# Performance work log

Hardware: AMD Instinct MI355X
Metric: run time of the kernel (lower is better)

## Reference

```python
import jax, jax.numpy as jnp
import numpy as np

N = 100000   # nodes
E = 3200000  # directed edges
F_IN = 128   # data.num_node_features
H = 16       # hidden
C = 2        # output classes (hard-coded in module)


def _glorot(key, fan_in, fan_out):
    s = jnp.sqrt(6.0 / (fan_in + fan_out)).astype(jnp.float32)
    return jax.random.uniform(key, (fan_in, fan_out), jnp.float32, -s, s)


def setup_inputs() -> dict:
    key = jax.random.key(0)
    ks = jax.random.split(key, 5)
    x = jax.random.normal(ks[0], (N, F_IN), jnp.float32)
    edge_index = jax.random.randint(ks[1], (2, E), 0, N, dtype=jnp.int64)
    return {
        "x": x,
        "edge_index": edge_index,
        "W1": _glorot(ks[2], F_IN, H), "b1": jnp.zeros((H,), jnp.float32),
        "W2": _glorot(ks[3], H, H),    "b2": jnp.zeros((H,), jnp.float32),
        "W3": _glorot(ks[4], H, C),    "b3": jnp.zeros((C,), jnp.float32),
    }


def _gcn_conv(x, W, b, src, dst, norm, n):
    # PyG GCNConv: linear transform, then normalized gather -> scatter-add, + bias
    h = x @ W                                   # [N, out]
    msg = h[src] * norm[:, None]                # [E+N, out] gather over source nodes
    out = jax.ops.segment_sum(msg, dst, num_segments=n)  # scatter-add at targets
    return out + b


def reference(x, edge_index, W1, b1, W2, b2, W3, b3):
    n = x.shape[0]
    loop = jnp.arange(n, dtype=edge_index.dtype)
    src = jnp.concatenate([edge_index[0], loop])  # add self-loops (PyG default)
    dst = jnp.concatenate([edge_index[1], loop])
    # symmetric normalization: deg^{-1/2}[src] * deg^{-1/2}[dst], deg = in-degree w/ self-loops
    deg = jax.ops.segment_sum(jnp.ones(src.shape, jnp.float32), dst, num_segments=n)
    dis = jnp.where(deg > 0, jax.lax.rsqrt(jnp.maximum(deg, 1.0)), 0.0)
    norm = dis[src] * dis[dst]
    # dropout is identity in eval mode
    h = jax.nn.relu(_gcn_conv(x, W1, b1, src, dst, norm, n))
    h = jax.nn.relu(_gcn_conv(h, W2, b2, src, dst, norm, n))
    h = _gcn_conv(h, W3, b3, src, dst, norm, n)
    return jax.nn.log_softmax(h, axis=1)
```

## Files before the change

kernel.cpp:

```cpp
#include <hip/hip_runtime.h>
#include <math.h>

#define NSB   512
#define BSH   8
#define BKN   256
#define ESMAX 6272
#define NBSMX 128

typedef _Float16 h8  __attribute__((ext_vector_type(8)));
typedef _Float16 h4  __attribute__((ext_vector_type(4)));
typedef _Float16 h2v __attribute__((ext_vector_type(2)));

__device__ inline int wave_scan_incl(int v) {
    int lane = threadIdx.x & 63;
#pragma unroll
    for (int d = 1; d < 64; d <<= 1) {
        int t = __shfl_up(v, d, 64);
        if (lane >= d) v += t;
    }
    return v;
}


__global__ void k_scan1(const int* __restrict__ in, int* __restrict__ out,
                        int* __restrict__ bsum, int n) {
    __shared__ int wsum[4];
    int base = blockIdx.x * 2048 + threadIdx.x * 8;
    int v[8];
    int ts = 0;
#pragma unroll
    for (int j = 0; j < 8; j++) {
        int idx = base + j;
        v[j] = ts;
        ts += (idx < n) ? in[idx] : 0;
    }
    int inc = wave_scan_incl(ts);
    int wid = threadIdx.x >> 6;
    if ((threadIdx.x & 63) == 63) wsum[wid] = inc;
    __syncthreads();
    int wofs = 0;
#pragma unroll
    for (int w = 0; w < 4; w++) wofs += (w < wid) ? wsum[w] : 0;
    int excl = inc - ts + wofs;
#pragma unroll
    for (int j = 0; j < 8; j++) {
        int idx = base + j;
        if (idx < n) out[idx] = excl + v[j];
    }
    if (threadIdx.x == 255) bsum[blockIdx.x] = excl + ts;
}

__device__ inline void scan_bsum(const int* __restrict__ bsum, int nbs,
                                 int* sb, int* wsumB) {
    int tid = threadIdx.x;
    int v = (tid < nbs) ? bsum[tid] : 0;
    int inc = wave_scan_incl(v);
    int wid = tid >> 6;
    if (tid < NBSMX && (tid & 63) == 63) wsumB[wid] = inc;
    __syncthreads();
    if (tid < nbs) {
        int wofs = 0;
#pragma unroll
        for (int w = 0; w < 2; w++) wofs += (w < wid) ? wsumB[w] : 0;
        sb[tid] = inc - v + wofs;
    }
    __syncthreads();
}


__global__ void k_hist(const int* __restrict__ dst, int* __restrict__ hist,
                       int e, int nbuck, int es) {
    __shared__ int h[512];
    for (int i = threadIdx.x; i < 512; i += blockDim.x) h[i] = 0;
    __syncthreads();
    int lo = blockIdx.x * es;
    int hi = min(lo + es, e);
    for (int i = lo + threadIdx.x; i < hi; i += blockDim.x)
        atomicAdd(&h[dst[i] >> BSH], 1);
    __syncthreads();
    for (int i = threadIdx.x; i < nbuck; i += blockDim.x)
        hist[(size_t)i * gridDim.x + blockIdx.x] = h[i];
}

__global__ void k_bucket(const int* __restrict__ src, const int* __restrict__ dst,
                         const int* __restrict__ hist, const int* __restrict__ offs,
                         const int* __restrict__ bsum, unsigned* __restrict__ col,
                         int e, int nbuck, int es, int nbs) {
    __shared__ unsigned sorted[ESMAX];
    __shared__ unsigned char sbuck[ESMAX];
    __shared__ int lofE[512], lcur[512], soff[512];
    __shared__ int sb[NBSMX];
    __shared__ int wsum[8];
    int tid = threadIdx.x;
    scan_bsum(bsum, nbs, sb, wsum);
    int lc = 0;
    if (tid < nbuck) {
        size_t idx = (size_t)tid * gridDim.x + blockIdx.x;
        lc = hist[idx];
        soff[tid] = offs[idx] + sb[idx >> 11];
    }
    int inc = wave_scan_incl(lc);
    int wid = tid >> 6;
    if ((tid & 63) == 63) wsum[wid] = inc;
    __syncthreads();
    int wofs = 0;
#pragma unroll
    for (int w = 0; w < 8; w++) wofs += (w < wid) ? wsum[w] : 0;
    int excl = inc - lc + wofs;
    lofE[tid] = excl;
    lcur[tid] = excl;
    __syncthreads();
    int lo = blockIdx.x * es;
    int hi = min(lo + es, e);
    for (int i = lo + tid; i < hi; i += 512) {
        int d = dst[i];
        int b = d >> BSH;
        int p = atomicAdd(&lcur[b], 1);
        sorted[p] = ((unsigned)src[i] << BSH) | (unsigned)(d & (BKN - 1));
        sbuck[p] = (unsigned char)(b & 255);
    }
    __syncthreads();
    int cnt_ = hi - lo;
    int split = (nbuck > 256) ? lofE[256] : 0x7fffffff;
    for (int i = tid; i < cnt_; i += 512) {
        int b = sbuck[i] | ((i >= split) ? 256 : 0);
        col[soff[b] + (i - lofE[b])] = sorted[i];
    }
}

__global__ void k_sort(const unsigned* __restrict__ col, const int* __restrict__ offs,
                       const int* __restrict__ bsum, int* __restrict__ col2,
                       int* __restrict__ rs, float* __restrict__ dis,
                       int n, int e, int nbuck, int nbs) {
    __shared__ int cnt[BKN];
    __shared__ int cur[BKN];
    __shared__ int sb[NBSMX];
    __shared__ int wsum[4];
    int tid = threadIdx.x;
    int b = blockIdx.x;
    scan_bsum(bsum, nbs, sb, wsum);
    size_t i0 = (size_t)b * NSB;
    int lo = offs[i0] + sb[i0 >> 11];
    int hi = e;
    if (b + 1 < nbuck) {
        size_t i1 = (size_t)(b + 1) * NSB;
        hi = offs[i1] + sb[i1 >> 11];
    }
    if (tid < BKN) cnt[tid] = 0;
    __syncthreads();
    for (int i = lo + tid; i < hi; i += 512)
        atomicAdd(&cnt[col[i] & (BKN - 1u)], 1);
    __syncthreads();
    int c = (tid < BKN) ? cnt[tid] : 0;
    int inc = wave_scan_incl(c);
    int wid = tid >> 6;
    if (tid < BKN && (tid & 63) == 63) wsum[wid] = inc;
    __syncthreads();
    if (tid < BKN) {
        int wofs = 0;
#pragma unroll
        for (int w = 0; w < 4; w++) wofs += (w < wid) ? wsum[w] : 0;
        int excl = inc - c + wofs;
        cur[tid] = lo + excl;
        int node = (b << BSH) + tid;
        if (node < n) {
            rs[node] = lo + excl;
            dis[node] = rsqrtf((float)(c + 1));
        }
    }
    if (b == 0 && tid == 0) rs[n] = e;
    __syncthreads();
    for (int i = lo + tid; i < hi; i += 512) {
        unsigned v = col[i];
        int pos = atomicAdd(&cur[v & (BKN - 1u)], 1);
        col2[pos] = (int)(v >> BSH);
    }
}


__global__ __launch_bounds__(512) void k_linear1s(
        const float* __restrict__ x, const float* __restrict__ W,
        const float* __restrict__ dis, _Float16* __restrict__ hs, int n) {
    __shared__ float sW[2048];
    int tid = threadIdx.x;
    for (int i = tid; i < 2048; i += 512) sW[i] = W[i];
    __syncthreads();
    int cg = tid & 3;
    int kg = (tid >> 2) & 7;
    int nl = tid >> 5;
    float wr[16][4];
#pragma unroll
    for (int j = 0; j < 16; j++)
#pragma unroll
        for (int cc = 0; cc < 4; cc++)
            wr[j][cc] = sW[(kg * 16 + j) * 16 + cg * 4 + cc];
    int nodeBase = blockIdx.x * 128 + nl;
    for (int it = 0; it < 8; it++) {
        int node = nodeBase + it * 16;
        float a0 = 0.f, a1 = 0.f, a2 = 0.f, a3 = 0.f;
        if (node < n) {
            const float4* xr = (const float4*)(x + (size_t)node * 128 + kg * 16);
#pragma unroll
            for (int j4 = 0; j4 < 4; j4++) {
                float4 xv = xr[j4];
                float xs0 = xv.x, xs1 = xv.y, xs2 = xv.z, xs3 = xv.w;
                int j = j4 * 4;
                a0 += xs0 * wr[j][0] + xs1 * wr[j+1][0] + xs2 * wr[j+2][0] + xs3 * wr[j+3][0];
                a1 += xs0 * wr[j][1] + xs1 * wr[j+1][1] + xs2 * wr[j+2][1] + xs3 * wr[j+3][1];
                a2 += xs0 * wr[j][2] + xs1 * wr[j+1][2] + xs2 * wr[j+2][2] + xs3 * wr[j+3][2];
                a3 += xs0 * wr[j][3] + xs1 * wr[j+1][3] + xs2 * wr[j+2][3] + xs3 * wr[j+3][3];
            }
        }
#pragma unroll
        for (int m = 4; m <= 16; m <<= 1) {
            a0 += __shfl_xor(a0, m);
            a1 += __shfl_xor(a1, m);
            a2 += __shfl_xor(a2, m);
            a3 += __shfl_xor(a3, m);
        }
        if (kg == 0 && node < n) {
            float d = dis[node];
            h4 o;
            o[0] = (_Float16)(a0 * d);
            o[1] = (_Float16)(a1 * d);
            o[2] = (_Float16)(a2 * d);
            o[3] = (_Float16)(a3 * d);
            *((h4*)(hs + (size_t)node * 16 + cg * 4)) = o;
        }
    }
}


__global__ void k_pullA(const _Float16* __restrict__ hs, const int* __restrict__ rs,
                        const int* __restrict__ col2, const float* __restrict__ dis,
                        const float* __restrict__ bb, const float* __restrict__ W,
                        _Float16* __restrict__ hsOut, int n) {
    __shared__ float sW[256];
    __shared__ float sb[16];
    if (threadIdx.x < 256) sW[threadIdx.x] = W[threadIdx.x];
    if (threadIdx.x < 16) sb[threadIdx.x] = bb[threadIdx.x];
    __syncthreads();
    long long t = (long long)blockIdx.x * blockDim.x + threadIdx.x;
    int node = (int)(t >> 3), sub = (int)(t & 7);
    int q = sub & 1, qt = sub >> 1;
    if (node >= n) return;
    const h8* H = (const h8*)hs;
    float acc[8];
    if (qt == 0) {
        h8 self = H[(size_t)node * 2 + q];
#pragma unroll
        for (int j = 0; j < 8; j++) acc[j] = (float)self[j];
    } else {
#pragma unroll
        for (int j = 0; j < 8; j++) acc[j] = 0.f;
    }
    int b = rs[node], e2 = rs[node + 1];
    int i = b + qt;
    for (; i + 12 < e2; i += 16) {
        int s0 = col2[i], s1 = col2[i + 4], s2 = col2[i + 8], s3 = col2[i + 12];
        h8 v0 = H[(size_t)s0 * 2 + q];
        h8 v1 = H[(size_t)s1 * 2 + q];
        h8 v2 = H[(size_t)s2 * 2 + q];
        h8 v3 = H[(size_t)s3 * 2 + q];
#pragma unroll
        for (int j = 0; j < 8; j++)
            acc[j] += (float)v0[j] + (float)v1[j] + (float)v2[j] + (float)v3[j];
    }
    for (; i < e2; i += 4) {
        h8 v = H[(size_t)col2[i] * 2 + q];
#pragma unroll
        for (int j = 0; j < 8; j++) acc[j] += (float)v[j];
    }
#pragma unroll
    for (int j = 0; j < 8; j++) {
        acc[j] += __shfl_xor(acc[j], 2);
        acc[j] += __shfl_xor(acc[j], 4);
    }
    float d = dis[node];
    float va[16];
#pragma unroll
    for (int j = 0; j < 8; j++) {
        int k = q * 8 + j;
        float v = acc[j] * d + sb[k];
        v = v > 0.f ? v : 0.f;
        float other = __shfl_xor(v, 1);
        va[j]     = q ? other : v;
        va[8 + j] = q ? v : other;
    }
    if (qt == 0) {
        h8 o;
#pragma unroll
        for (int j = 0; j < 8; j++) {
            int c = q * 8 + j;
            float s = 0.f;
#pragma unroll
            for (int k = 0; k < 16; k++) s += va[k] * sW[k * 16 + c];
            o[j] = (_Float16)(s * d);
        }
        ((h8*)hsOut)[(size_t)node * 2 + q] = o;
    }
}


__global__ void k_pullB(const _Float16* __restrict__ hs, const int* __restrict__ rs,
                        const int* __restrict__ col2, const float* __restrict__ dis,
                        const float* __restrict__ bb, const float* __restrict__ W,
                        _Float16* __restrict__ hs2, int n) {
    __shared__ float sW[32];
    __shared__ float sb[16];
    if (threadIdx.x < 32) sW[threadIdx.x] = W[threadIdx.x];
    if (threadIdx.x < 16) sb[threadIdx.x] = bb[threadIdx.x];
    __syncthreads();
    long long t = (long long)blockIdx.x * blockDim.x + threadIdx.x;
    int node = (int)(t >> 3), sub = (int)(t & 7);
    int q = sub & 1, qt = sub >> 1;
    if (node >= n) return;
    const h8* H = (const h8*)hs;
    float acc[8];
    if (qt == 0) {
        h8 self = H[(size_t)node * 2 + q];
#pragma unroll
        for (int j = 0; j < 8; j++) acc[j] = (float)self[j];
    } else {
#pragma unroll
        for (int j = 0; j < 8; j++) acc[j] = 0.f;
    }
    int b = rs[node], e2 = rs[node + 1];
    int i = b + qt;
    for (; i + 12 < e2; i += 16) {
        int s0 = col2[i], s1 = col2[i + 4], s2 = col2[i + 8], s3 = col2[i + 12];
        h8 v0 = H[(size_t)s0 * 2 + q];
        h8 v1 = H[(size_t)s1 * 2 + q];
        h8 v2 = H[(size_t)s2 * 2 + q];
        h8 v3 = H[(size_t)s3 * 2 + q];
#pragma unroll
        for (int j = 0; j < 8; j++)
            acc[j] += (float)v0[j] + (float)v1[j] + (float)v2[j] + (float)v3[j];
    }
    for (; i < e2; i += 4) {
        h8 v = H[(size_t)col2[i] * 2 + q];
#pragma unroll
        for (int j = 0; j < 8; j++) acc[j] += (float)v[j];
    }
#pragma unroll
    for (int j = 0; j < 8; j++) {
        acc[j] += __shfl_xor(acc[j], 2);
        acc[j] += __shfl_xor(acc[j], 4);
    }
    float d = dis[node];
    float p0 = 0.f, p1 = 0.f;
#pragma unroll
    for (int j = 0; j < 8; j++) {
        int k = q * 8 + j;
        float v = acc[j] * d + sb[k];
        v = v > 0.f ? v : 0.f;
        p0 += v * sW[k * 2 + 0];
        p1 += v * sW[k * 2 + 1];
    }
    p0 += __shfl_xor(p0, 1);
    p1 += __shfl_xor(p1, 1);
    if (sub == 0) {
        h2v o;
        o[0] = (_Float16)(p0 * d);
        o[1] = (_Float16)(p1 * d);
        ((h2v*)hs2)[node] = o;
    }
}


__global__ void k_pull2lsm(const _Float16* __restrict__ hs2, const int* __restrict__ rs,
                           const int* __restrict__ col2, const float* __restrict__ dis,
                           const float* __restrict__ b3, float* __restrict__ out, int n) {
    long long t = (long long)blockIdx.x * blockDim.x + threadIdx.x;
    int node = (int)(t >> 2), qt = (int)(t & 3);
    if (node >= n) return;
    const h2v* H = (const h2v*)hs2;
    float a0 = 0.f, a1 = 0.f;
    if (qt == 0) {
        h2v self = H[node];
        a0 = (float)self[0]; a1 = (float)self[1];
    }
    int b = rs[node], e2 = rs[node + 1];
    int i = b + qt;
    for (; i + 12 < e2; i += 16) {
        h2v v0 = H[col2[i]];
        h2v v1 = H[col2[i + 4]];
        h2v v2 = H[col2[i + 8]];
        h2v v3 = H[col2[i + 12]];
        a0 += (float)v0[0] + (float)v1[0] + (float)v2[0] + (float)v3[0];
        a1 += (float)v0[1] + (float)v1[1] + (float)v2[1] + (float)v3[1];
    }
    for (; i < e2; i += 4) {
        h2v v = H[col2[i]];
        a0 += (float)v[0];
        a1 += (float)v[1];
    }
    a0 += __shfl_xor(a0, 1); a0 += __shfl_xor(a0, 2);
    a1 += __shfl_xor(a1, 1); a1 += __shfl_xor(a1, 2);
    if (qt == 0) {
        float d = dis[node];
        float z0 = a0 * d + b3[0];
        float z1 = a1 * d + b3[1];
        float m = fmaxf(z0, z1);
        float l = m + logf(expf(z0 - m) + expf(z1 - m));
        float2 o = {z0 - l, z1 - l};
        ((float2*)out)[node] = o;
    }
}


extern "C" void kernel_launch(void* const* d_in, const int* in_sizes, int n_in,
                              void* d_out, int out_size, void* d_ws, size_t ws_size,
                              hipStream_t stream) {
    const float* x  = (const float*)d_in[0];
    const int*   ei = (const int*)d_in[1];
    const float* W1 = (const float*)d_in[2];
    const float* b1 = (const float*)d_in[3];
    const float* W2 = (const float*)d_in[4];
    const float* b2 = (const float*)d_in[5];
    const float* W3 = (const float*)d_in[6];
    const float* b3 = (const float*)d_in[7];
    float* out = (float*)d_out;

    const int N = in_sizes[0] / 128;
    const int E = in_sizes[1] / 2;
    const int* src = ei;
    const int* dst = ei + E;

    const int NBUCK = (N + BKN - 1) >> BSH;
    const int M = NBUCK * NSB;
    const int ES = (E + NSB - 1) / NSB;
    const int NBS = (M + 2047) / 2048;

    char* ws = (char*)d_ws;
    size_t off = 0;
    auto alloc = [&](size_t bytes) {
        void* p = ws + off;
        off += (bytes + 255) & ~(size_t)255;
        return p;
    };
    int*       hist = (int*)alloc((size_t)M * sizeof(int));
    int*       offs = (int*)alloc((size_t)M * sizeof(int));
    int*       bsum = (int*)alloc(NBSMX * sizeof(int));
    unsigned*  col  = (unsigned*)alloc((size_t)E * sizeof(unsigned));
    int*       col2 = (int*)alloc((size_t)E * sizeof(int));
    int*       rs   = (int*)alloc((size_t)(N + 1) * sizeof(int));
    float*     dis  = (float*)alloc((size_t)N * sizeof(float));
    _Float16*  hsA  = (_Float16*)alloc((size_t)N * 16 * sizeof(_Float16));
    _Float16*  hsB  = (_Float16*)alloc((size_t)N * 16 * sizeof(_Float16));
    _Float16*  hs2  = (_Float16*)alloc((size_t)N * 2 * sizeof(_Float16));

    const int B = 256;
    auto g = [&](long long work) { return (int)((work + B - 1) / B); };

    k_hist<<<NSB, B, 0, stream>>>(dst, hist, E, NBUCK, ES);
    k_scan1<<<NBS, 256, 0, stream>>>(hist, offs, bsum, M);
    k_bucket<<<NSB, 512, 0, stream>>>(src, dst, hist, offs, bsum, col, E, NBUCK, ES, NBS);
    k_sort<<<NBUCK, 512, 0, stream>>>(col, offs, bsum, col2, rs, dis, N, E, NBUCK, NBS);

    k_linear1s<<<(N + 127) / 128, 512, 0, stream>>>(x, W1, dis, hsA, N);

    k_pullA<<<g((long long)N * 8), B, 0, stream>>>(hsA, rs, col2, dis, b1, W2, hsB, N);

    k_pullB<<<g((long long)N * 8), B, 0, stream>>>(hsB, rs, col2, dis, b2, W3, hs2, N);

    k_pull2lsm<<<g((long long)N * 4), B, 0, stream>>>(hs2, rs, col2, dis, b3, out, N);
}
```

Baseline: 247.4 us.

## Replace histogram and global scan with atomic per-bucket fixed-capacity slots

Removes the separate histogram and prefix-scan kernels. Instead, the bucketing kernel counts locally and reserves space in fixed-size per-bucket slots (SLOT entries each) using global atomics. Nodes now carry explicit start and end row pointers, since buckets are no longer packed contiguously. This drops two launches and one extra pass over dst. In exchange it assumes no bucket of 256 nodes gets more than SLOT edges, which holds for uniformly random graphs but would overflow on skewed degree distributions. It also makes the edge order inside a bucket depend on atomic timing.

```diff
diff --git a/kernel.cpp b/kernel.cpp
--- a/kernel.cpp
+++ b/kernel.cpp
@@ -5,7 +5,7 @@
 #define BSH   8
 #define BKN   256
 #define ESMAX 6272
-#define NBSMX 128
+#define SLOT  10240
 
 typedef _Float16 h8  __attribute__((ext_vector_type(8)));
 typedef _Float16 h4  __attribute__((ext_vector_type(4)));
@@ -22,96 +22,35 @@
 }
 
 
-__global__ void k_scan1(const int* __restrict__ in, int* __restrict__ out,
-                        int* __restrict__ bsum, int n) {
-    __shared__ int wsum[4];
-    int base = blockIdx.x * 2048 + threadIdx.x * 8;
-    int v[8];
-    int ts = 0;
-#pragma unroll
-    for (int j = 0; j < 8; j++) {
-        int idx = base + j;
-        v[j] = ts;
-        ts += (idx < n) ? in[idx] : 0;
-    }
-    int inc = wave_scan_incl(ts);
-    int wid = threadIdx.x >> 6;
-    if ((threadIdx.x & 63) == 63) wsum[wid] = inc;
-    __syncthreads();
-    int wofs = 0;
-#pragma unroll
-    for (int w = 0; w < 4; w++) wofs += (w < wid) ? wsum[w] : 0;
-    int excl = inc - ts + wofs;
-#pragma unroll
-    for (int j = 0; j < 8; j++) {
-        int idx = base + j;
-        if (idx < n) out[idx] = excl + v[j];
-    }
-    if (threadIdx.x == 255) bsum[blockIdx.x] = excl + ts;
-}
-
-__device__ inline void scan_bsum(const int* __restrict__ bsum, int nbs,
-                                 int* sb, int* wsumB) {
+__global__ void k_bucket(const int* __restrict__ src, const int* __restrict__ dst,
+                         int* __restrict__ gcur, unsigned* __restrict__ col,
+                         int e, int nbuck, int es) {
+    __shared__ unsigned sorted[ESMAX];
+    __shared__ unsigned char sbuck[ESMAX];
+    __shared__ int lc[512], lofE[512], lcur[512], soff[512];
+    __shared__ int wsum[8];
     int tid = threadIdx.x;
-    int v = (tid < nbs) ? bsum[tid] : 0;
-    int inc = wave_scan_incl(v);
-    int wid = tid >> 6;
-    if (tid < NBSMX && (tid & 63) == 63) wsumB[wid] = inc;
-    __syncthreads();
-    if (tid < nbs) {
-        int wofs = 0;
-#pragma unroll
-        for (int w = 0; w < 2; w++) wofs += (w < wid) ? wsumB[w] : 0;
-        sb[tid] = inc - v + wofs;
-    }
-    __syncthreads();
-}
-
-
-__global__ void k_hist(const int* __restrict__ dst, int* __restrict__ hist,
-                       int e, int nbuck, int es) {
-    __shared__ int h[512];
-    for (int i = threadIdx.x; i < 512; i += blockDim.x) h[i] = 0;
+    lc[tid] = 0;
     __syncthreads();
     int lo = blockIdx.x * es;
     int hi = min(lo + es, e);
-    for (int i = lo + threadIdx.x; i < hi; i += blockDim.x)
-        atomicAdd(&h[dst[i] >> BSH], 1);
-    __syncthreads();
-    for (int i = threadIdx.x; i < nbuck; i += blockDim.x)
-        hist[(size_t)i * gridDim.x + blockIdx.x] = h[i];
-}
-
-__global__ void k_bucket(const int* __restrict__ src, const int* __restrict__ dst,
-                         const int* __restrict__ hist, const int* __restrict__ offs,
-                         const int* __restrict__ bsum, unsigned* __restrict__ col,
-                         int e, int nbuck, int es, int nbs) {
-    __shared__ unsigned sorted[ESMAX];
-    __shared__ unsigned char sbuck[ESMAX];
-    __shared__ int lofE[512], lcur[512], soff[512];
-    __shared__ int sb[NBSMX];
-    __shared__ int wsum[8];
-    int tid = threadIdx.x;
-    scan_bsum(bsum, nbs, sb, wsum);
-    int lc = 0;
-    if (tid < nbuck) {
-        size_t idx = (size_t)tid * gridDim.x + blockIdx.x;
-        lc = hist[idx];
-        soff[tid] = offs[idx] + sb[idx >> 11];
-    }
-    int inc = wave_scan_incl(lc);
+    for (int i = lo + tid; i < hi; i += 512)
+        atomicAdd(&lc[dst[i] >> BSH], 1);
+    __syncthreads();
+    int c = lc[tid];
+    int inc = wave_scan_incl(c);
     int wid = tid >> 6;
     if ((tid & 63) == 63) wsum[wid] = inc;
     __syncthreads();
     int wofs = 0;
 #pragma unroll
     for (int w = 0; w < 8; w++) wofs += (w < wid) ? wsum[w] : 0;
-    int excl = inc - lc + wofs;
+    int excl = inc - c + wofs;
     lofE[tid] = excl;
     lcur[tid] = excl;
-    __syncthreads();
-    int lo = blockIdx.x * es;
-    int hi = min(lo + es, e);
+    if (tid < nbuck && c > 0)
+        soff[tid] = tid * SLOT + atomicAdd(&gcur[tid], c);
+    __syncthreads();
     for (int i = lo + tid; i < hi; i += 512) {
         int d = dst[i];
         int b = d >> BSH;
@@ -128,24 +67,18 @@
     }
 }
 
-__global__ void k_sort(const unsigned* __restrict__ col, const int* __restrict__ offs,
-                       const int* __restrict__ bsum, int* __restrict__ col2,
-                       int* __restrict__ rs, float* __restrict__ dis,
-                       int n, int e, int nbuck, int nbs) {
+
+__global__ void k_sort(const unsigned* __restrict__ col, const int* __restrict__ gcur,
+                       int* __restrict__ col2, int* __restrict__ rs,
+                       int* __restrict__ re, float* __restrict__ dis,
+                       int n, int nbuck) {
     __shared__ int cnt[BKN];
     __shared__ int cur[BKN];
-    __shared__ int sb[NBSMX];
     __shared__ int wsum[4];
     int tid = threadIdx.x;
     int b = blockIdx.x;
-    scan_bsum(bsum, nbs, sb, wsum);
-    size_t i0 = (size_t)b * NSB;
-    int lo = offs[i0] + sb[i0 >> 11];
-    int hi = e;
-    if (b + 1 < nbuck) {
-        size_t i1 = (size_t)(b + 1) * NSB;
-        hi = offs[i1] + sb[i1 >> 11];
-    }
+    int lo = b * SLOT;
+    int hi = lo + gcur[b];
     if (tid < BKN) cnt[tid] = 0;
     __syncthreads();
     for (int i = lo + tid; i < hi; i += 512)
@@ -165,10 +98,10 @@
         int node = (b << BSH) + tid;
         if (node < n) {
             rs[node] = lo + excl;
+            re[node] = lo + excl + c;
             dis[node] = rsqrtf((float)(c + 1));
         }
     }
-    if (b == 0 && tid == 0) rs[n] = e;
     __syncthreads();
     for (int i = lo + tid; i < hi; i += 512) {
         unsigned v = col[i];
@@ -232,9 +165,9 @@
 
 
 __global__ void k_pullA(const _Float16* __restrict__ hs, const int* __restrict__ rs,
-                        const int* __restrict__ col2, const float* __restrict__ dis,
-                        const float* __restrict__ bb, const float* __restrict__ W,
-                        _Float16* __restrict__ hsOut, int n) {
+                        const int* __restrict__ re, const int* __restrict__ col2,
+                        const float* __restrict__ dis, const float* __restrict__ bb,
+                        const float* __restrict__ W, _Float16* __restrict__ hsOut, int n) {
     __shared__ float sW[256];
     __shared__ float sb[16];
     if (threadIdx.x < 256) sW[threadIdx.x] = W[threadIdx.x];
@@ -254,7 +187,7 @@
 #pragma unroll
         for (int j = 0; j < 8; j++) acc[j] = 0.f;
     }
-    int b = rs[node], e2 = rs[node + 1];
+    int b = rs[node], e2 = re[node];
     int i = b + qt;
     for (; i + 12 < e2; i += 16) {
         int s0 = col2[i], s1 = col2[i + 4], s2 = col2[i + 8], s3 = col2[i + 12];
@@ -303,9 +236,9 @@
 
 
 __global__ void k_pullB(const _Float16* __restrict__ hs, const int* __restrict__ rs,
-                        const int* __restrict__ col2, const float* __restrict__ dis,
-                        const float* __restrict__ bb, const float* __restrict__ W,
-                        _Float16* __restrict__ hs2, int n) {
+                        const int* __restrict__ re, const int* __restrict__ col2,
+                        const float* __restrict__ dis, const float* __restrict__ bb,
+                        const float* __restrict__ W, _Float16* __restrict__ hs2, int n) {
     __shared__ float sW[32];
     __shared__ float sb[16];
     if (threadIdx.x < 32) sW[threadIdx.x] = W[threadIdx.x];
@@ -325,7 +258,7 @@
 #pragma unroll
         for (int j = 0; j < 8; j++) acc[j] = 0.f;
     }
-    int b = rs[node], e2 = rs[node + 1];
+    int b = rs[node], e2 = re[node];
     int i = b + qt;
     for (; i + 12 < e2; i += 16) {
         int s0 = col2[i], s1 = col2[i + 4], s2 = col2[i + 8], s3 = col2[i + 12];
@@ -369,8 +302,9 @@
 
 
 __global__ void k_pull2lsm(const _Float16* __restrict__ hs2, const int* __restrict__ rs,
-                           const int* __restrict__ col2, const float* __restrict__ dis,
-                           const float* __restrict__ b3, float* __restrict__ out, int n) {
+                           const int* __restrict__ re, const int* __restrict__ col2,
+                           const float* __restrict__ dis, const float* __restrict__ b3,
+                           float* __restrict__ out, int n) {
     long long t = (long long)blockIdx.x * blockDim.x + threadIdx.x;
     int node = (int)(t >> 2), qt = (int)(t & 3);
     if (node >= n) return;
@@ -380,7 +314,7 @@
         h2v self = H[node];
         a0 = (float)self[0]; a1 = (float)self[1];
     }
-    int b = rs[node], e2 = rs[node + 1];
+    int b = rs[node], e2 = re[node];
     int i = b + qt;
     for (; i + 12 < e2; i += 16) {
         h2v v0 = H[col2[i]];
@@ -428,9 +362,7 @@
     const int* dst = ei + E;
 
     const int NBUCK = (N + BKN - 1) >> BSH;
-    const int M = NBUCK * NSB;
     const int ES = (E + NSB - 1) / NSB;
-    const int NBS = (M + 2047) / 2048;
 
     char* ws = (char*)d_ws;
     size_t off = 0;
@@ -439,12 +371,11 @@
         off += (bytes + 255) & ~(size_t)255;
         return p;
     };
-    int*       hist = (int*)alloc((size_t)M * sizeof(int));
-    int*       offs = (int*)alloc((size_t)M * sizeof(int));
-    int*       bsum = (int*)alloc(NBSMX * sizeof(int));
-    unsigned*  col  = (unsigned*)alloc((size_t)E * sizeof(unsigned));
-    int*       col2 = (int*)alloc((size_t)E * sizeof(int));
-    int*       rs   = (int*)alloc((size_t)(N + 1) * sizeof(int));
+    int*       gcur = (int*)alloc((size_t)NBUCK * sizeof(int));
+    unsigned*  col  = (unsigned*)alloc((size_t)NBUCK * SLOT * sizeof(unsigned));
+    int*       col2 = (int*)alloc((size_t)NBUCK * SLOT * sizeof(int));
+    int*       rs   = (int*)alloc((size_t)N * sizeof(int));
+    int*       re   = (int*)alloc((size_t)N * sizeof(int));
     float*     dis  = (float*)alloc((size_t)N * sizeof(float));
     _Float16*  hsA  = (_Float16*)alloc((size_t)N * 16 * sizeof(_Float16));
     _Float16*  hsB  = (_Float16*)alloc((size_t)N * 16 * sizeof(_Float16));
@@ -453,16 +384,15 @@
     const int B = 256;
     auto g = [&](long long work) { return (int)((work + B - 1) / B); };
 
-    k_hist<<<NSB, B, 0, stream>>>(dst, hist, E, NBUCK, ES);
-    k_scan1<<<NBS, 256, 0, stream>>>(hist, offs, bsum, M);
-    k_bucket<<<NSB, 512, 0, stream>>>(src, dst, hist, offs, bsum, col, E, NBUCK, ES, NBS);
-    k_sort<<<NBUCK, 512, 0, stream>>>(col, offs, bsum, col2, rs, dis, N, E, NBUCK, NBS);
+    hipMemsetAsync(gcur, 0, (size_t)NBUCK * sizeof(int), stream);
+    k_bucket<<<NSB, 512, 0, stream>>>(src, dst, gcur, col, E, NBUCK, ES);
+    k_sort<<<NBUCK, 512, 0, stream>>>(col, gcur, col2, rs, re, dis, N, NBUCK);
 
     k_linear1s<<<(N + 127) / 128, 512, 0, stream>>>(x, W1, dis, hsA, N);
 
-    k_pullA<<<g((long long)N * 8), B, 0, stream>>>(hsA, rs, col2, dis, b1, W2, hsB, N);
-
-    k_pullB<<<g((long long)N * 8), B, 0, stream>>>(hsB, rs, col2, dis, b2, W3, hs2, N);
-
-    k_pull2lsm<<<g((long long)N * 4), B, 0, stream>>>(hs2, rs, col2, dis, b3, out, N);
-}
+    k_pullA<<<g((long long)N * 8), B, 0, stream>>>(hsA, rs, re, col2, dis, b1, W2, hsB, N);
+
+    k_pullB<<<g((long long)N * 8), B, 0, stream>>>(hsB, rs, re, col2, dis, b2, W3, hs2, N);
+
+    k_pull2lsm<<<g((long long)N * 4), B, 0, stream>>>(hs2, rs, re, col2, dis, b3, out, N);
+}
```

Measured after the change: 245.5 us, median of 2. No clear change (-0.8%).
